# Kernel tuning notes

Measured on AMD Instinct MI355X. Metric: run time of the kernel, lower is better.

Reference implementation:

```python
import jax, jax.numpy as jnp
import numpy as np
from jax import lax

B, L, D = 8, 2048, 512


def _mlp(x, w1, w2):
    # MemoryMLP: x + gelu(x @ w1) @ w2  (exact gelu, matching F.gelu default)
    return x + jax.nn.gelu(x @ w1, approximate=False) @ w2


def _l2norm(t):
    # F.normalize(p=2, dim=-1, eps=1e-12)
    n = jnp.linalg.norm(t, axis=-1, keepdims=True)
    return t / jnp.maximum(n, 1e-12)


def setup_inputs() -> dict:
    key = jax.random.key(0)
    ks = jax.random.split(key, 12)
    s = 0.02
    return {
        "x": jax.random.normal(ks[0], (B, L, D), jnp.float32),
        "conv_w": jax.random.normal(ks[1], (D, 1, 4), jnp.float32) * s,  # depthwise, (out, in/groups, k)
        "conv_b": jax.random.normal(ks[2], (D,), jnp.float32) * s,
        "q_w": jax.random.normal(ks[3], (D, D), jnp.float32) * s,  # Linear weight (out, in)
        "mem_w1": jax.random.normal(ks[4], (D, D), jnp.float32) * s,
        "mem_w2": jax.random.normal(ks[5], (D, D), jnp.float32) * s,
        "eta_w1": jax.random.normal(ks[6], (D, D), jnp.float32) * s,
        "eta_w2": jax.random.normal(ks[7], (D, D), jnp.float32) * s,
        "alpha_w1": jax.random.normal(ks[8], (D, D), jnp.float32) * s,
        "alpha_w2": jax.random.normal(ks[9], (D, D), jnp.float32) * s,
    }


def _forward(x, conv_w, conv_b, q_w, mem_w1, mem_w2, eta_w1, eta_w2, alpha_w1, alpha_w2):
    # causal depthwise conv: Conv1d(k=4, padding=3, groups=D) then slice [:L] == left-pad 3
    xc = lax.conv_general_dilated(
        jnp.transpose(x, (0, 2, 1)),  # (B, D, L)
        conv_w,                        # (D, 1, 4)
        window_strides=(1,),
        padding=[(3, 0)],
        feature_group_count=D,
        dimension_numbers=("NCH", "OIH", "NCH"),
    ) + conv_b[None, :, None]
    xc = jnp.transpose(xc, (0, 2, 1))  # (B, L, D)

    # time-invariant branches (m_k/m_v weights are never updated; kt/vt/hat_v do not
    # affect the output, so they are elided). q, eta, alpha use fixed weights -> vectorize.
    q = _l2norm(xc @ q_w.T)                                   # (B, L, D)
    eta_mean = jax.nn.sigmoid(_mlp(xc, eta_w1, eta_w2)).mean(axis=(0, 2))      # (L,)
    alpha_mean = jax.nn.sigmoid(_mlp(xc, alpha_w1, alpha_w2)).mean(axis=(0, 2))  # (L,)

    def step(carry, inp):
        w1, w2 = carry
        q_t, a_t, e_t = inp  # (B, D), (), ()
        o_t = _mlp(q_t, w1, w2)  # output uses pre-update memory
        new_w1 = w1 * a_t - e_t * 0.01
        new_w2 = w2 * a_t - e_t * 0.01
        return (new_w1, new_w2), o_t

    qs = jnp.transpose(q, (1, 0, 2))  # (L, B, D)
    (_, _), outs = lax.scan(step, (mem_w1, mem_w2), (qs, alpha_mean, eta_mean))
    return jnp.transpose(outs, (1, 0, 2))  # (B, L, D)


def reference(x, conv_w, conv_b, q_w, mem_w1, mem_w2, eta_w1, eta_w2, alpha_w1, alpha_w2):
    return _forward(x, conv_w, conv_b, q_w, mem_w1, mem_w2, eta_w1, eta_w2, alpha_w1, alpha_w2)
```

## Files before the change

### kernel.cpp

```cpp
#include <hip/hip_runtime.h>
#include <math.h>

constexpr int Bn = 8, Ln = 2048, Dn = 512;
constexpr int Mn = Bn * Ln;
constexpr int CONV_BLOCKS = Mn * Dn / 16 / 256;
constexpr int WPREP_BLOCKS = 448;
constexpr int ZERO_FLOATS = 3 * Mn + 2 * Ln;
constexpr int ZERO_BLOCKS = ZERO_FLOATS / (256 * 4);

typedef __bf16 bf16x8 __attribute__((ext_vector_type(8)));
typedef __bf16 bf16x4v __attribute__((ext_vector_type(4)));
typedef float f32x4 __attribute__((ext_vector_type(4)));

__device__ __forceinline__ float sigmoid_fast(float x) {
    return __builtin_amdgcn_rcpf(1.0f + __expf(-x));
}
__device__ __forceinline__ float gelu_fast(float x) {
    return x * sigmoid_fast(1.5957691216f * (x + 0.044715f * x * x * x));
}

__global__ __launch_bounds__(256) void prep_kernel(
    const float* __restrict__ x, const float* __restrict__ w,
    const float* __restrict__ bias, __bf16* __restrict__ xcb,
    const float* __restrict__ ew1, const float* __restrict__ aw1,
    const float* __restrict__ ew2, const float* __restrict__ aw2,
    const float* __restrict__ mw1, const float* __restrict__ mw2,
    const float* __restrict__ qw,
    __bf16* __restrict__ Wall, __bf16* __restrict__ W2t,
    __bf16* __restrict__ m1t, __bf16* __restrict__ m2t,
    float* __restrict__ zero_zone) {
    __shared__ float tile[64][65];
    if (blockIdx.x < CONV_BLOCKS) {
        int idx = blockIdx.x * 256 + threadIdx.x;
        int g = idx & 127;
        int r4 = idx >> 7;
        int bl0 = r4 * 4;
        int l0 = bl0 & (Ln - 1);
        int d = g * 4;
        float4 b4 = *(const float4*)&bias[d];
        float wv[16];
        *(float4*)&wv[0]  = *(const float4*)&w[d * 4];
        *(float4*)&wv[4]  = *(const float4*)&w[d * 4 + 4];
        *(float4*)&wv[8]  = *(const float4*)&w[d * 4 + 8];
        *(float4*)&wv[12] = *(const float4*)&w[d * 4 + 12];
        float4 xv[7];
#pragma unroll
        for (int t = 0; t < 7; ++t) {
            int ll = l0 - 3 + t;
            xv[t] = (ll >= 0) ? *(const float4*)&x[(size_t)(bl0 - 3 + t) * Dn + d]
                              : make_float4(0.f, 0.f, 0.f, 0.f);
        }
#pragma unroll
        for (int i = 0; i < 4; ++i) {
            float a0 = b4.x, a1 = b4.y, a2 = b4.z, a3 = b4.w;
#pragma unroll
            for (int k = 0; k < 4; ++k) {
                float4 xt = xv[i + k];
                a0 += xt.x * wv[0 * 4 + k];
                a1 += xt.y * wv[1 * 4 + k];
                a2 += xt.z * wv[2 * 4 + k];
                a3 += xt.w * wv[3 * 4 + k];
            }
            bf16x4v o = { (__bf16)a0, (__bf16)a1, (__bf16)a2, (__bf16)a3 };
            *(bf16x4v*)&xcb[(size_t)(bl0 + i) * Dn + d] = o;
        }
        return;
    }
    if (blockIdx.x >= CONV_BLOCKS + WPREP_BLOCKS) {
        int idx = (blockIdx.x - CONV_BLOCKS - WPREP_BLOCKS) * 256 + threadIdx.x;
        ((float4*)zero_zone)[idx] = make_float4(0.f, 0.f, 0.f, 0.f);
        return;
    }
    int bid = blockIdx.x - CONV_BLOCKS;
    int z = bid >> 6;
    int t = bid & 63;
    int r0 = (t >> 3) * 64, c0 = (t & 7) * 64;
    const float* src;
    __bf16* dst;
    int trans = 1;
    switch (z) {
        case 0: src = ew1; dst = Wall; break;
        case 1: src = aw1; dst = Wall + 512 * 512; break;
        case 2: src = ew2; dst = W2t; break;
        case 3: src = aw2; dst = W2t + 512 * 512; break;
        case 4: src = mw1; dst = m1t; break;
        case 5: src = mw2; dst = m2t; break;
        default: src = qw; dst = Wall + 1024 * 512; trans = 0; break;
    }
    if (!trans) {
        for (int i = threadIdx.x; i < 4096; i += 256) {
            int r = i >> 6, c = i & 63;
            dst[(size_t)(r0 + r) * 512 + c0 + c] = (__bf16)src[(size_t)(r0 + r) * 512 + c0 + c];
        }
        return;
    }
    for (int i = threadIdx.x; i < 4096; i += 256) {
        int r = i >> 6, c = i & 63;
        tile[r][c] = src[(size_t)(r0 + r) * 512 + c0 + c];
    }
    __syncthreads();
    for (int i = threadIdx.x; i < 4096; i += 256) {
        int r = i >> 6, c = i & 63;
        dst[(size_t)(c0 + r) * 512 + r0 + c] = (__bf16)tile[c][r];
    }
}

template <int OP, int BM>
__global__ __launch_bounds__(256, 4) void gemm_mfma(
    const __bf16* __restrict__ A, int lda, int Az,
    const __bf16* __restrict__ Bt, int Bz,
    void* __restrict__ C0, void* __restrict__ C1,
    const __bf16* __restrict__ auxb,
    const float* __restrict__ Pv, const float* __restrict__ Qv,
    const float* __restrict__ SSv, const float* __restrict__ RSv,
    float* __restrict__ red0, float* __restrict__ red1, float* __restrict__ red2) {
    constexpr int MI = BM / 32;
    constexpr int AISS = BM / 32;
    constexpr int ACH = BM * 4;
    __shared__ __align__(16) __bf16 Asl[BM * 64];
    __shared__ __align__(16) __bf16 Bsl[128 * 64];
    const int tid = threadIdx.x;
    const int lane = tid & 63, wv = tid >> 6;
    const int wm = wv & 1, wn = wv >> 1;
    const int fr = lane & 15, fq = lane >> 4;
    const int z = blockIdx.z;
    A += (size_t)z * Az;
    Bt += (size_t)z * Bz;
    const __bf16* Ab = A + (size_t)blockIdx.y * BM * lda;
    const __bf16* Bb = Bt + (size_t)blockIdx.x * 128 * 512;
    float* redp = (OP == 1) ? red0 + (size_t)z * Ln : red0;

    f32x4 acc[MI][4] = {};

    for (int k0 = 0; k0 < 512; k0 += 64) {
#pragma unroll
        for (int i = 0; i < AISS; ++i) {
            int c = tid + i * 256;
            int s = c / ACH;
            int cl = c - s * ACH;
            int r = cl >> 2, co = (cl & 3) * 8 + s * 32;
            __builtin_amdgcn_global_load_lds(
                (const __attribute__((address_space(1))) void*)(Ab + (size_t)r * lda + k0 + co),
                (__attribute__((address_space(3))) void*)(Asl + c * 8), 16, 0, 0);
        }
#pragma unroll
        for (int i = 0; i < 4; ++i) {
            int c = tid + i * 256;
            int s = c >> 9;
            int cl = c & 511;
            int r = cl >> 2, co = (cl & 3) * 8 + s * 32;
            __builtin_amdgcn_global_load_lds(
                (const __attribute__((address_space(1))) void*)(Bb + (size_t)r * 512 + k0 + co),
                (__attribute__((address_space(3))) void*)(Bsl + c * 8), 16, 0, 0);
        }
        __syncthreads();
#pragma unroll
        for (int ks = 0; ks < 2; ++ks) {
            bf16x8 af[MI], bfr[4];
#pragma unroll
            for (int mi = 0; mi < MI; ++mi)
                af[mi] = *(const bf16x8*)&Asl[ks * BM * 32 +
                                              (wm * (BM / 2) + mi * 16 + fr) * 32 + fq * 8];
#pragma unroll
            for (int ni = 0; ni < 4; ++ni)
                bfr[ni] = *(const bf16x8*)&Bsl[ks * 4096 +
                                               (wn * 64 + ni * 16 + fr) * 32 + fq * 8];
#pragma unroll
            for (int mi = 0; mi < MI; ++mi)
#pragma unroll
                for (int ni = 0; ni < 4; ++ni)
                    acc[mi][ni] = __builtin_amdgcn_mfma_f32_16x16x32_bf16(
                        af[mi], bfr[ni], acc[mi][ni], 0, 0, 0);
        }
        __syncthreads();
    }

    const int row_base = blockIdx.y * BM + wm * (BM / 2);
    const int col_base = blockIdx.x * 128 + wn * 64;
    const bool qpath = (OP == 0) && (blockIdx.x >= 8);
#pragma unroll
    for (int mi = 0; mi < MI; ++mi) {
#pragma unroll
        for (int r = 0; r < 4; ++r) {
            int row = row_base + mi * 16 + fq * 4 + r;
            float p = 0.f, qs = 0.f, rs = 0.f, inv = 1.f;
            if (OP >= 3) {
                int t = row & (Ln - 1);
                p = Pv[t]; qs = Qv[t];
                rs = RSv[row];
                inv = 1.0f / fmaxf(sqrtf(SSv[row]), 1e-12f);
            }
            float s1 = 0.f, s2 = 0.f;
#pragma unroll
            for (int ni = 0; ni < 4; ++ni) {
                int col = col_base + ni * 16 + fr;
                float v = acc[mi][ni][r];
                if (OP == 0) {
                    if (!qpath) {
                        v = gelu_fast(v);
                        ((__bf16*)C0)[(size_t)row * 1024 + col] = (__bf16)v;
                    } else {
                        ((__bf16*)C1)[(size_t)row * 512 + col - 1024] = (__bf16)v;
                        s1 += v; s2 += v * v;
                    }
                } else if (OP == 1) {
                    v = sigmoid_fast((float)auxb[(size_t)row * 512 + col] + v);
                    s1 += v;
                } else if (OP == 3) {
                    v = gelu_fast(inv * (p * v + qs * rs));
                    ((__bf16*)C0)[(size_t)row * 512 + col] = (__bf16)v;
                    s1 += v;
                } else if (OP == 4) {
                    float qn = (float)auxb[(size_t)row * 512 + col] * inv;
                    ((float*)C0)[(size_t)row * 512 + col] = qn + p * v + qs * rs;
                }
            }
            if (OP == 1 || OP == 3 || (OP == 0 && qpath)) {
                s1 += __shfl_xor(s1, 1, 64);
                s1 += __shfl_xor(s1, 2, 64);
                s1 += __shfl_xor(s1, 4, 64);
                s1 += __shfl_xor(s1, 8, 64);
                if (OP == 0) {
                    s2 += __shfl_xor(s2, 1, 64);
                    s2 += __shfl_xor(s2, 2, 64);
                    s2 += __shfl_xor(s2, 4, 64);
                    s2 += __shfl_xor(s2, 8, 64);
                }
                if (fr == 0) {
                    if (OP == 1) atomicAdd(&redp[row & (Ln - 1)], s1 * (1.0f / 4096.0f));
                    else if (OP == 3) atomicAdd(&red0[row], s1);
                    else { atomicAdd(&red1[row], s2); atomicAdd(&red2[row], s1); }
                }
            }
        }
    }
}

__global__ __launch_bounds__(256) void scan_kernel(const float* __restrict__ a,
                                                   const float* __restrict__ e,
                                                   float* __restrict__ P,
                                                   float* __restrict__ Q) {
    int tid = threadIdx.x;
    int base = tid * 8;
    float la[8], le[8], Aloc[8], Bloc[8];
#pragma unroll
    for (int j = 0; j < 8; ++j) { la[j] = a[base + j]; le[j] = e[base + j]; }
    float Ac = 1.f, Bc = 0.f;
#pragma unroll
    for (int j = 0; j < 8; ++j) {
        Aloc[j] = Ac; Bloc[j] = Bc;
        Bc = Bc * la[j] - 0.01f * le[j];
        Ac *= la[j];
    }
    float Aw = Ac, Bw = Bc;
#pragma unroll
    for (int off = 1; off < 64; off <<= 1) {
        float Ap = __shfl_up(Aw, off, 64);
        float Bp = __shfl_up(Bw, off, 64);
        if ((tid & 63) >= off) { Bw = Aw * Bp + Bw; Aw = Aw * Ap; }
    }
    __shared__ float wA[4], wB[4];
    if ((tid & 63) == 63) { wA[tid >> 6] = Aw; wB[tid >> 6] = Bw; }
    __syncthreads();
    float Apre = 1.f, Bpre = 0.f;
    for (int w = 0; w < (tid >> 6); ++w) { Bpre = wA[w] * Bpre + wB[w]; Apre = wA[w] * Apre; }
    float Ax = __shfl_up(Aw, 1, 64), Bx = __shfl_up(Bw, 1, 64);
    if ((tid & 63) == 0) { Ax = 1.f; Bx = 0.f; }
    float At = Ax * Apre, Bt2 = Ax * Bpre + Bx;
#pragma unroll
    for (int j = 0; j < 8; ++j) {
        P[base + j] = Aloc[j] * At;
        Q[base + j] = Aloc[j] * Bt2 + Bloc[j];
    }
}

extern "C" void kernel_launch(void* const* d_in, const int* in_sizes, int n_in,
                              void* d_out, int out_size, void* d_ws, size_t ws_size,
                              hipStream_t stream) {
    const float* x        = (const float*)d_in[0];
    const float* conv_w   = (const float*)d_in[1];
    const float* conv_b   = (const float*)d_in[2];
    const float* q_w      = (const float*)d_in[3];
    const float* mem_w1   = (const float*)d_in[4];
    const float* mem_w2   = (const float*)d_in[5];
    const float* eta_w1   = (const float*)d_in[6];
    const float* eta_w2   = (const float*)d_in[7];
    const float* alpha_w1 = (const float*)d_in[8];
    const float* alpha_w2 = (const float*)d_in[9];
    float* out = (float*)d_out;

    char* w = (char*)d_ws;
    __bf16* xcb  = (__bf16*)w;    w += (size_t)Mn * Dn * 2;
    __bf16* H    = (__bf16*)w;    w += (size_t)Mn * 1024 * 2;
    __bf16* qb   = (__bf16*)w;    w += (size_t)Mn * Dn * 2;
    __bf16* G    = (__bf16*)w;    w += (size_t)Mn * Dn * 2;
    __bf16* Wall = (__bf16*)w;    w += (size_t)1536 * 512 * 2;
    __bf16* W2t  = (__bf16*)w;    w += (size_t)2 * 512 * 512 * 2;
    __bf16* m1t  = (__bf16*)w;    w += (size_t)512 * 512 * 2;
    __bf16* m2t  = (__bf16*)w;    w += (size_t)512 * 512 * 2;
    float* Rv      = (float*)w;   w += (size_t)Mn * 4;
    float* MeanAcc = (float*)w;   w += (size_t)2 * Ln * 4;
    float* SS      = (float*)w;   w += (size_t)Mn * 4;
    float* RS      = (float*)w;   w += (size_t)Mn * 4;
    float* Pv = (float*)w;        w += Ln * 4;
    float* Qv = (float*)w;        w += Ln * 4;

    prep_kernel<<<CONV_BLOCKS + WPREP_BLOCKS + ZERO_BLOCKS, 256, 0, stream>>>(
        x, conv_w, conv_b, xcb, eta_w1, alpha_w1, eta_w2, alpha_w2,
        mem_w1, mem_w2, q_w, Wall, W2t, m1t, m2t, Rv);
    gemm_mfma<0, 128><<<dim3(12, 128), 256, 0, stream>>>(
        xcb, 512, 0, Wall, 0, H, qb, nullptr,
        nullptr, nullptr, nullptr, nullptr, nullptr, SS, RS);
    gemm_mfma<1, 128><<<dim3(4, 128, 2), 256, 0, stream>>>(
        H, 1024, 512, W2t, 512 * 512, nullptr, nullptr, xcb,
        nullptr, nullptr, nullptr, nullptr, MeanAcc, nullptr, nullptr);
    scan_kernel<<<1, 256, 0, stream>>>(MeanAcc + Ln, MeanAcc, Pv, Qv);
    gemm_mfma<3, 64><<<dim3(4, 256), 256, 0, stream>>>(
        qb, 512, 0, m1t, 0, G, nullptr, nullptr,
        Pv, Qv, SS, RS, Rv, nullptr, nullptr);
    gemm_mfma<4, 64><<<dim3(4, 256), 256, 0, stream>>>(
        G, 512, 0, m2t, 0, out, nullptr, qb,
        Pv, Qv, SS, Rv, nullptr, nullptr, nullptr);
}
```

Measured before the change: 227.5 us.

## Replace 4-wave GEMM blocks with single-wave 64x64 tiles and XCD-aware block mapping

New measurement: 254.8 us. 1.12x slower.

```diff
diff --git a/kernel.cpp b/kernel.cpp
--- a/kernel.cpp
+++ b/kernel.cpp
@@ -105,8 +105,8 @@
     }
 }
 
-template <int OP, int BM>
-__global__ __launch_bounds__(256, 4) void gemm_mfma(
+template <int OP, int NX>
+__global__ __launch_bounds__(64, 4) void gemm_w(
     const __bf16* __restrict__ A, int lda, int Az,
     const __bf16* __restrict__ Bt, int Bz,
     void* __restrict__ C0, void* __restrict__ C1,
@@ -114,72 +114,63 @@
     const float* __restrict__ Pv, const float* __restrict__ Qv,
     const float* __restrict__ SSv, const float* __restrict__ RSv,
     float* __restrict__ red0, float* __restrict__ red1, float* __restrict__ red2) {
-    constexpr int MI = BM / 32;
-    constexpr int AISS = BM / 32;
-    constexpr int ACH = BM * 4;
-    __shared__ __align__(16) __bf16 Asl[BM * 64];
-    __shared__ __align__(16) __bf16 Bsl[128 * 64];
-    const int tid = threadIdx.x;
-    const int lane = tid & 63, wv = tid >> 6;
-    const int wm = wv & 1, wn = wv >> 1;
+    __shared__ __align__(16) __bf16 Asl[64 * 32];
+    __shared__ __align__(16) __bf16 Bsl[64 * 32];
+    const int lane = threadIdx.x;
     const int fr = lane & 15, fq = lane >> 4;
+    const int id = blockIdx.x;
+    const int xcd = id & 7;
+    const int i2 = id >> 3;
+    const int bx = i2 % NX;
+    const int by = (xcd << 5) + i2 / NX;
     const int z = blockIdx.z;
     A += (size_t)z * Az;
     Bt += (size_t)z * Bz;
-    const __bf16* Ab = A + (size_t)blockIdx.y * BM * lda;
-    const __bf16* Bb = Bt + (size_t)blockIdx.x * 128 * 512;
+    const __bf16* Ab = A + (size_t)by * 64 * lda;
+    const __bf16* Bb = Bt + (size_t)bx * 64 * 512;
     float* redp = (OP == 1) ? red0 + (size_t)z * Ln : red0;
 
-    f32x4 acc[MI][4] = {};
-
-    for (int k0 = 0; k0 < 512; k0 += 64) {
-#pragma unroll
-        for (int i = 0; i < AISS; ++i) {
-            int c = tid + i * 256;
-            int s = c / ACH;
-            int cl = c - s * ACH;
-            int r = cl >> 2, co = (cl & 3) * 8 + s * 32;
+    f32x4 acc[4][4] = {};
+
+    for (int k0 = 0; k0 < 512; k0 += 32) {
+#pragma unroll
+        for (int i = 0; i < 4; ++i) {
+            int c = lane + i * 64;
+            int r = c >> 2, co = (c & 3) * 8;
             __builtin_amdgcn_global_load_lds(
                 (const __attribute__((address_space(1))) void*)(Ab + (size_t)r * lda + k0 + co),
                 (__attribute__((address_space(3))) void*)(Asl + c * 8), 16, 0, 0);
         }
 #pragma unroll
         for (int i = 0; i < 4; ++i) {
-            int c = tid + i * 256;
-            int s = c >> 9;
-            int cl = c & 511;
-            int r = cl >> 2, co = (cl & 3) * 8 + s * 32;
+            int c = lane + i * 64;
+            int r = c >> 2, co = (c & 3) * 8;
             __builtin_amdgcn_global_load_lds(
                 (const __attribute__((address_space(1))) void*)(Bb + (size_t)r * 512 + k0 + co),
                 (__attribute__((address_space(3))) void*)(Bsl + c * 8), 16, 0, 0);
         }
         __syncthreads();
-#pragma unroll
-        for (int ks = 0; ks < 2; ++ks) {
-            bf16x8 af[MI], bfr[4];
-#pragma unroll
-            for (int mi = 0; mi < MI; ++mi)
-                af[mi] = *(const bf16x8*)&Asl[ks * BM * 32 +
-                                              (wm * (BM / 2) + mi * 16 + fr) * 32 + fq * 8];
+        bf16x8 af[4], bfr[4];
+#pragma unroll
+        for (int mi = 0; mi < 4; ++mi)
+            af[mi] = *(const bf16x8*)&Asl[(mi * 16 + fr) * 32 + fq * 8];
+#pragma unroll
+        for (int ni = 0; ni < 4; ++ni)
+            bfr[ni] = *(const bf16x8*)&Bsl[(ni * 16 + fr) * 32 + fq * 8];
+#pragma unroll
+        for (int mi = 0; mi < 4; ++mi)
 #pragma unroll
             for (int ni = 0; ni < 4; ++ni)
-                bfr[ni] = *(const bf16x8*)&Bsl[ks * 4096 +
-                                               (wn * 64 + ni * 16 + fr) * 32 + fq * 8];
-#pragma unroll
-            for (int mi = 0; mi < MI; ++mi)
-#pragma unroll
-                for (int ni = 0; ni < 4; ++ni)
-                    acc[mi][ni] = __builtin_amdgcn_mfma_f32_16x16x32_bf16(
-                        af[mi], bfr[ni], acc[mi][ni], 0, 0, 0);
-        }
+                acc[mi][ni] = __builtin_amdgcn_mfma_f32_16x16x32_bf16(
+                    af[mi], bfr[ni], acc[mi][ni], 0, 0, 0);
         __syncthreads();
     }
 
-    const int row_base = blockIdx.y * BM + wm * (BM / 2);
-    const int col_base = blockIdx.x * 128 + wn * 64;
-    const bool qpath = (OP == 0) && (blockIdx.x >= 8);
-#pragma unroll
-    for (int mi = 0; mi < MI; ++mi) {
+    const int row_base = by * 64;
+    const int col_base = bx * 64;
+    const bool qpath = (OP == 0) && (bx >= 16);
+#pragma unroll
+    for (int mi = 0; mi < 4; ++mi) {
 #pragma unroll
         for (int r = 0; r < 4; ++r) {
             int row = row_base + mi * 16 + fq * 4 + r;
@@ -308,17 +299,17 @@
     prep_kernel<<<CONV_BLOCKS + WPREP_BLOCKS + ZERO_BLOCKS, 256, 0, stream>>>(
         x, conv_w, conv_b, xcb, eta_w1, alpha_w1, eta_w2, alpha_w2,
         mem_w1, mem_w2, q_w, Wall, W2t, m1t, m2t, Rv);
-    gemm_mfma<0, 128><<<dim3(12, 128), 256, 0, stream>>>(
+    gemm_w<0, 24><<<24 * 256, 64, 0, stream>>>(
         xcb, 512, 0, Wall, 0, H, qb, nullptr,
         nullptr, nullptr, nullptr, nullptr, nullptr, SS, RS);
-    gemm_mfma<1, 128><<<dim3(4, 128, 2), 256, 0, stream>>>(
+    gemm_w<1, 8><<<dim3(8 * 256, 1, 2), 64, 0, stream>>>(
         H, 1024, 512, W2t, 512 * 512, nullptr, nullptr, xcb,
         nullptr, nullptr, nullptr, nullptr, MeanAcc, nullptr, nullptr);
     scan_kernel<<<1, 256, 0, stream>>>(MeanAcc + Ln, MeanAcc, Pv, Qv);
-    gemm_mfma<3, 64><<<dim3(4, 256), 256, 0, stream>>>(
+    gemm_w<3, 8><<<8 * 256, 64, 0, stream>>>(
         qb, 512, 0, m1t, 0, G, nullptr, nullptr,
         Pv, Qv, SS, RS, Rv, nullptr, nullptr);
-    gemm_mfma<4, 64><<<dim3(4, 256), 256, 0, stream>>>(
+    gemm_w<4, 8><<<8 * 256, 64, 0, stream>>>(
         G, 512, 0, m2t, 0, out, nullptr, qb,
         Pv, Qv, SS, Rv, nullptr, nullptr, nullptr);
 }
```
